# Performance work log

Measured on AMD Instinct MI355X. Metric: run time of the kernel, lower is better.

## Reference

```python
import jax, jax.numpy as jnp
import numpy as np

B, N, DIM, H, HD, COND, BS = 2, 1024, 768, 12, 64, 128, 16
S = 2 * N  # noised tokens [0:N) concatenated with clean x0 tokens [N:2N)
EPS = 1e-5
NEG = -1e30


def setup_inputs() -> dict:
    key = jax.random.key(0)
    ks = jax.random.split(key, 8)
    d = {}
    d['x'] = jax.random.normal(ks[0], (B, S, DIM), jnp.float32)
    d['c'] = jax.random.normal(ks[1], (B, COND), jnp.float32)
    # Rotary table for positions 0..N-1 (each half of the 2N sequence reuses the same positions)
    inv_freq = 1.0 / (10000.0 ** (np.arange(0, HD, 2, dtype=np.float64) / HD))
    freqs = np.arange(N, dtype=np.float64)[:, None] * inv_freq[None, :]
    emb = np.concatenate([freqs, freqs], axis=-1)  # [N, HD]
    cos = np.tile(np.cos(emb), (2, 1))[None, :, None, None, :]
    sin = np.tile(np.sin(emb), (2, 1))[None, :, None, None, :]
    d['cos'] = jnp.asarray(cos, jnp.float32)
    d['sin'] = jnp.asarray(sin, jnp.float32)
    # block-causal diffusion mask (flex_attention_mask): same (block, x0-flag) OR
    # cross-attention from noised block q>0 to strictly earlier CLEAN (x0) blocks
    idx = np.arange(S)
    fl = (idx >= N).astype(np.int64)
    blk = np.where(fl == 1, (idx - N) // BS, idx // BS)
    same = (blk[:, None] == blk[None, :]) & (fl[:, None] == fl[None, :])
    allowed = (blk[:, None] > 0) & (blk[None, :] < blk[:, None]) & (fl[None, :] == 1)
    d['mask'] = jnp.asarray(same | allowed)
    # parameters (adaLN is zero-init in the source; randomized here so the block is non-trivial)
    w = 0.02
    d['norm1_w'] = jnp.ones((DIM,), jnp.float32)
    d['qkv_w'] = jax.random.normal(ks[2], (3 * DIM, DIM), jnp.float32) * w
    d['attn_out_w'] = jax.random.normal(ks[3], (DIM, DIM), jnp.float32) * w
    d['norm2_w'] = jnp.ones((DIM,), jnp.float32)
    d['mlp_w1'] = jax.random.normal(ks[4], (4 * DIM, DIM), jnp.float32) * w
    d['mlp_b1'] = jnp.zeros((4 * DIM,), jnp.float32)
    d['mlp_w2'] = jax.random.normal(ks[5], (DIM, 4 * DIM), jnp.float32) * w
    d['mlp_b2'] = jnp.zeros((DIM,), jnp.float32)
    d['adaLN_w'] = jax.random.normal(ks[6], (6 * DIM, COND), jnp.float32) * w
    d['adaLN_b'] = jax.random.normal(ks[7], (6 * DIM,), jnp.float32) * w
    return d


def _ln(x, w):
    # F.layer_norm (no bias) followed by learned scale, as in the custom LayerNorm
    mu = x.mean(-1, keepdims=True)
    xc = x - mu
    var = (xc * xc).mean(-1, keepdims=True)
    return xc * jax.lax.rsqrt(var + EPS) * w


def reference(x, c, cos, sin, mask, norm1_w, qkv_w, attn_out_w, norm2_w,
              mlp_w1, mlp_b1, mlp_w2, mlp_b2, adaLN_w, adaLN_b):
    # adaLN modulation: [B, 6*DIM] -> six [B, 1, DIM] chunks
    mods = c @ adaLN_w.T + adaLN_b
    (shift_msa, scale_msa, gate_msa,
     shift_mlp, scale_mlp, gate_mlp) = jnp.split(mods[:, None, :], 6, axis=-1)
    x_skip = x
    h = _ln(x, norm1_w) * (1.0 + scale_msa) + shift_msa  # modulate_fused
    # qkv projection + rotary (torchscript path: qkv*cos + rotate_half(qkv)*sin)
    qkv = (h @ qkv_w.T).reshape(x.shape[0], S, 3, H, HD)
    rot = jnp.concatenate([-qkv[..., HD // 2:], qkv[..., :HD // 2]], axis=-1)
    qkv = qkv * cos + rot * sin
    q, k, v = qkv[:, :, 0], qkv[:, :, 1], qkv[:, :, 2]
    # SDPA with the block-causal diffusion mask, scale 1/sqrt(head_dim)
    scores = jnp.einsum('bqhd,bkhd->bhqk', q, k) / np.sqrt(HD).astype(np.float32)
    scores = jnp.where(mask[None, None], scores, NEG)
    p = jax.nn.softmax(scores, axis=-1)
    a = jnp.einsum('bhqk,bkhd->bqhd', p, v).reshape(x.shape[0], S, DIM)
    # bias_dropout_add_scale (inference => no dropout): gate * attn_out + residual
    x = gate_msa * (a @ attn_out_w.T) + x_skip
    h2 = _ln(x, norm2_w) * (1.0 + scale_mlp) + shift_mlp
    m = jax.nn.gelu(h2 @ mlp_w1.T + mlp_b1, approximate=True) @ mlp_w2.T + mlp_b2
    return x + gate_mlp * m
```

## Files before the change

### kernel.cpp

```cpp
#include <hip/hip_runtime.h>
#include <hip/hip_bf16.h>

#define EPS 1e-5f

typedef __attribute__((ext_vector_type(8))) short bf16x8;
typedef __attribute__((ext_vector_type(4))) short bf16x4;
typedef __attribute__((ext_vector_type(4))) float f32x4;

__device__ __forceinline__ f32x4 mfma_bf16(bf16x8 a, bf16x8 b, f32x4 c) {
    return __builtin_amdgcn_mfma_f32_16x16x32_bf16(a, b, c, 0, 0, 0);
}

__device__ __forceinline__ void async_ld16(const void* g, void* l) {
    __builtin_amdgcn_global_load_lds(
        (const __attribute__((address_space(1))) void*)g,
        (__attribute__((address_space(3))) void*)l, 16, 0, 0);
}

__device__ __forceinline__ float fast_gelu(float v) {
    float z2 = 1.5957691216057308f * (v + 0.044715f * v * v * v);
    float e = __expf(z2);
    return v * e / (e + 1.f);
}

__device__ __forceinline__ float bf2f(short s) {
    union { float f; unsigned u; } v;
    v.u = ((unsigned)(unsigned short)s) << 16;
    return v.f;
}

__global__ void k_pre(const float* __restrict__ a, __hip_bfloat16* __restrict__ oa, int na,
                      const float* __restrict__ b, __hip_bfloat16* __restrict__ ob, int nb,
                      const float* __restrict__ c, __hip_bfloat16* __restrict__ oc, int nc,
                      const float* __restrict__ d, __hip_bfloat16* __restrict__ od, int nd,
                      const float* __restrict__ cond, const float* __restrict__ alw,
                      const float* __restrict__ alb, float* __restrict__ mods) {
    if (blockIdx.x >= 27648) {
        int i = (blockIdx.x - 27648) * 256 + threadIdx.x;
        int bb = i / 4608, row = i - bb * 4608;
        const float4* cv = (const float4*)(cond + bb * 128);
        const float4* wv = (const float4*)(alw + (long)row * 128);
        float acc = 0.f;
#pragma unroll
        for (int k = 0; k < 32; ++k) {
            float4 x = cv[k], y = wv[k];
            acc += x.x * y.x + x.y * y.y + x.z * y.z + x.w * y.w;
        }
        mods[i] = acc + alb[row];
        return;
    }
    int i = blockIdx.x * 256 + threadIdx.x;
    if (i < na) { oa[i] = __float2bfloat16(a[i]); return; }
    i -= na;
    if (i < nb) { ob[i] = __float2bfloat16(b[i]); return; }
    i -= nb;
    if (i < nc) { oc[i] = __float2bfloat16(c[i]); return; }
    i -= nc;
    if (i < nd) od[i] = __float2bfloat16(d[i]);
}

__global__ void k_ln_mod(const float* __restrict__ x, const float* __restrict__ w,
                         const float* __restrict__ mods, int shiftOff, int scaleOff,
                         __hip_bfloat16* __restrict__ out) {
    int token = blockIdx.x;
    int lane = threadIdx.x;
    const float4* xr = (const float4*)(x + (long)token * 768);
    float4 v0 = xr[lane], v1 = xr[lane + 64], v2 = xr[lane + 128];
    float s  = v0.x + v0.y + v0.z + v0.w + v1.x + v1.y + v1.z + v1.w + v2.x + v2.y + v2.z + v2.w;
    float ss = v0.x*v0.x + v0.y*v0.y + v0.z*v0.z + v0.w*v0.w
             + v1.x*v1.x + v1.y*v1.y + v1.z*v1.z + v1.w*v1.w
             + v2.x*v2.x + v2.y*v2.y + v2.z*v2.z + v2.w*v2.w;
#pragma unroll
    for (int m = 32; m >= 1; m >>= 1) { s += __shfl_xor(s, m); ss += __shfl_xor(ss, m); }
    float mu = s * (1.f / 768.f);
    float var = ss * (1.f / 768.f) - mu * mu;
    float rs = rsqrtf(var + EPS);
    int b = token >> 11;
    const float* sh = mods + b * 4608 + shiftOff;
    const float* sc = mods + b * 4608 + scaleOff;
    __hip_bfloat16* o = out + (long)token * 768;
    float4 vv[3] = {v0, v1, v2};
#pragma unroll
    for (int kk = 0; kk < 3; ++kk) {
        int cbase = (lane + 64 * kk) * 4;
        const float* p = (const float*)&vv[kk];
#pragma unroll
        for (int j = 0; j < 4; ++j) {
            int col = cbase + j;
            float hv = (p[j] - mu) * rs * w[col] * (1.f + sc[col]) + sh[col];
            o[col] = __float2bfloat16(hv);
        }
    }
}

__global__ void k_red(const __hip_bfloat16* __restrict__ p, const float* __restrict__ x2,
                      const float* __restrict__ mods, const float* __restrict__ bias,
                      float* __restrict__ out) {
    long base = ((long)blockIdx.x * 256 + threadIdx.x) * 4;
    int col = (int)(base % 768);
    int row = (int)(base / 768);
    int b = row >> 11;
    short4 a0 = *(const short4*)(p + base);
    short4 a1 = *(const short4*)(p + 3145728 + base);
    float4 xr = *(const float4*)(x2 + base);
    float4 gt = *(const float4*)(mods + b * 4608 + 3840 + col);
    float4 bs = *(const float4*)(bias + col);
    float4 o;
    o.x = xr.x + gt.x * (bf2f(a0.x) + bf2f(a1.x) + bs.x);
    o.y = xr.y + gt.y * (bf2f(a0.y) + bf2f(a1.y) + bs.y);
    o.z = xr.z + gt.z * (bf2f(a0.z) + bf2f(a1.z) + bs.z);
    o.w = xr.w + gt.w * (bf2f(a0.w) + bf2f(a1.w) + bs.w);
    *(float4*)(out + base) = o;
}

__global__ __launch_bounds__(256) void k_attn(
    const __hip_bfloat16* __restrict__ q, const __hip_bfloat16* __restrict__ k,
    const __hip_bfloat16* __restrict__ vT, __hip_bfloat16* __restrict__ out) {
    __shared__ __hip_bfloat16 pbuf[4][640];
    int wave = threadIdx.x >> 6;
    int lane = threadIdx.x & 63;
    int l15 = lane & 15, quad = lane >> 4;
    int bh = blockIdx.x >> 5;
    int pp = blockIdx.x & 31;
    int fl, blk;
    if      (wave == 0) { fl = 0; blk = 2 * pp; }
    else if (wave == 1) { fl = 0; blk = 2 * pp + 1; }
    else if (wave == 2) { fl = 1; blk = 63 - 2 * pp; }
    else                { fl = 1; blk = 62 - 2 * pp; }
    int qblk = fl * 64 + blk;

    const __hip_bfloat16* Q = q + ((long)bh * 2048 + qblk * 16) * 64;
    bf16x8 qa = *(const bf16x8*)(Q + l15 * 64 + quad * 8);
    bf16x8 qb = *(const bf16x8*)(Q + l15 * 64 + 32 + quad * 8);
    const __hip_bfloat16* K = k + (long)bh * 2048 * 64;
    const __hip_bfloat16* V = vT + (long)bh * 64 * 2048;
    __hip_bfloat16* P = &pbuf[wave][0];

    const f32x4 vzero = {0.f, 0.f, 0.f, 0.f};
    f32x4 o[4]; float l[4];
#pragma unroll
    for (int r = 0; r < 4; ++r) { o[r] = vzero; l[r] = 0.f; }

    int plen = (blk + fl) * 16;
    int nch = (plen + 31) >> 5;
    int total = nch + (fl ? 0 : 1);

    int kbase = (0 < nch) ? 1024 : blk * 16;
    bool v1 = (0 < nch) && (16 < plen);
    bf16x8 ka, kb, k1a, k1b;
    {
        const __hip_bfloat16* K0 = K + (long)kbase * 64;
        ka = *(const bf16x8*)(K0 + l15 * 64 + quad * 8);
        kb = *(const bf16x8*)(K0 + l15 * 64 + 32 + quad * 8);
        k1a = ka; k1b = kb;
        if (v1) {
            const __hip_bfloat16* K1 = K0 + 16 * 64;
            k1a = *(const bf16x8*)(K1 + l15 * 64 + quad * 8);
            k1b = *(const bf16x8*)(K1 + l15 * 64 + 32 + quad * 8);
        }
    }

    for (int ci = 0; ci < total; ++ci) {
        bf16x8 vf[4];
#pragma unroll
        for (int tt = 0; tt < 4; ++tt)
            vf[tt] = *(const bf16x8*)(V + (long)(tt * 16 + l15) * 2048 + kbase + quad * 8);

        f32x4 s0 = mfma_bf16(qb, kb, mfma_bf16(qa, ka, vzero));
        f32x4 s1 = vzero;
        if (v1) s1 = mfma_bf16(qb, k1b, mfma_bf16(qa, k1a, vzero));

        bool hasNext = (ci + 1) < total;
        int nkbase = kbase; bool nv1 = false;
        bf16x8 nka = ka, nkb = kb, nk1a = ka, nk1b = kb;
        if (hasNext) {
            nkbase = (ci + 1 < nch) ? 1024 + (ci + 1) * 32 : blk * 16;
            nv1 = (ci + 1 < nch) && ((ci + 1) * 32 + 16) < plen;
            const __hip_bfloat16* K0 = K + (long)nkbase * 64;
            nka = *(const bf16x8*)(K0 + l15 * 64 + quad * 8);
            nkb = *(const bf16x8*)(K0 + l15 * 64 + 32 + quad * 8);
            if (nv1) {
                const __hip_bfloat16* K1 = K0 + 16 * 64;
                nk1a = *(const bf16x8*)(K1 + l15 * 64 + quad * 8);
                nk1b = *(const bf16x8*)(K1 + l15 * 64 + 32 + quad * 8);
            }
        }

        float p0[4], p1[4];
#pragma unroll
        for (int r = 0; r < 4; ++r) p0[r] = __expf(s0[r]);
        if (v1) {
#pragma unroll
            for (int r = 0; r < 4; ++r) p1[r] = __expf(s1[r]);
        } else {
#pragma unroll
            for (int r = 0; r < 4; ++r) p1[r] = 0.f;
        }
#pragma unroll
        for (int r = 0; r < 4; ++r) {
            l[r] += p0[r] + p1[r];
            int row = quad * 4 + r;
            P[row * 36 + l15]      = __float2bfloat16(p0[r]);
            P[row * 36 + 16 + l15] = __float2bfloat16(p1[r]);
        }
        asm volatile("s_waitcnt lgkmcnt(0)" ::: "memory");
        union { bf16x4 h[2]; bf16x8 v; } u;
        u.h[0] = *(const bf16x4*)(P + l15 * 36 + quad * 8);
        u.h[1] = *(const bf16x4*)(P + l15 * 36 + quad * 8 + 4);
        bf16x8 pa = u.v;
#pragma unroll
        for (int tt = 0; tt < 4; ++tt) o[tt] = mfma_bf16(pa, vf[tt], o[tt]);
        asm volatile("s_waitcnt lgkmcnt(0)" ::: "memory");

        kbase = nkbase; v1 = nv1;
        ka = nka; kb = nkb; k1a = nk1a; k1b = nk1b;
    }

    int b = bh / 12, h = bh - b * 12;
    int seqbase = qblk * 16;
#pragma unroll
    for (int r = 0; r < 4; ++r) {
        float lr = l[r];
#pragma unroll
        for (int msk = 1; msk < 16; msk <<= 1) lr += __shfl_xor(lr, msk, 16);
        float inv = 1.f / lr;
        long row = b * 2048 + seqbase + quad * 4 + r;
#pragma unroll
        for (int tt = 0; tt < 4; ++tt)
            out[row * 768 + h * 64 + tt * 16 + l15] = __float2bfloat16(o[tt][r] * inv);
    }
}

__global__ __launch_bounds__(128) void k_gemm64(
    const __hip_bfloat16* __restrict__ A, const __hip_bfloat16* __restrict__ W,
    __hip_bfloat16* __restrict__ Cb, const float* __restrict__ bias,
    int M, int N, int K) {
    __shared__ __hip_bfloat16 lA[4][64 * 32];
    __shared__ __hip_bfloat16 lB[4][64 * 32];
    int t = threadIdx.x;
    int wave = t >> 6, lane = t & 63, l15 = lane & 15, quad = lane >> 4;
    int sw8 = (quad ^ ((l15 >> 1) & 3)) * 8;
    long bm = blockIdx.x, bn = blockIdx.y;
    const __hip_bfloat16* Ab = A + bm * 64 * K;
    const __hip_bfloat16* Wb = W + bn * 64 * K;

    long soff[2];
#pragma unroll
    for (int call = 0; call < 2; ++call) {
        int chunk = call * 128 + t;
        int row = chunk >> 2;
        int c = (chunk & 3) ^ ((row >> 1) & 3);
        soff[call] = (long)row * K + c * 8;
    }
    auto stage = [&](int k0, int buf) {
        char* lAc = (char*)&lA[buf][0];
        char* lBc = (char*)&lB[buf][0];
#pragma unroll
        for (int call = 0; call < 2; ++call) {
            async_ld16(Ab + soff[call] + k0, lAc + call * 2048 + wave * 1024);
            async_ld16(Wb + soff[call] + k0, lBc + call * 2048 + wave * 1024);
        }
    };

    f32x4 acc[2][4];
#pragma unroll
    for (int i = 0; i < 2; ++i)
#pragma unroll
        for (int j = 0; j < 4; ++j) acc[i][j] = (f32x4){0.f, 0.f, 0.f, 0.f};

    int nIter = K / 32;
    stage(0, 0);
    stage(32, 1);
    stage(64, 2);
    for (int i = 0; i < nIter; ++i) {
        int cb = i & 3;
        if (i > 0) asm volatile("s_barrier" ::: "memory");
        if (i + 3 < nIter) {
            stage((i + 3) * 32, (i + 3) & 3);
            asm volatile("s_waitcnt vmcnt(12)" ::: "memory");
        } else if (i + 3 == nIter) {
            asm volatile("s_waitcnt vmcnt(8)" ::: "memory");
        } else if (i + 2 == nIter) {
            asm volatile("s_waitcnt vmcnt(4)" ::: "memory");
        } else {
            asm volatile("s_waitcnt vmcnt(0)" ::: "memory");
        }
        asm volatile("s_barrier" ::: "memory");
        bf16x8 af[2], bfr[4];
#pragma unroll
        for (int ii = 0; ii < 2; ++ii)
            af[ii] = *(const bf16x8*)&lA[cb][(wave * 32 + ii * 16 + l15) * 32 + sw8];
#pragma unroll
        for (int j = 0; j < 4; ++j)
            bfr[j] = *(const bf16x8*)&lB[cb][(j * 16 + l15) * 32 + sw8];
#pragma unroll
        for (int ii = 0; ii < 2; ++ii)
#pragma unroll
            for (int j = 0; j < 4; ++j)
                acc[ii][j] = mfma_bf16(af[ii], bfr[j], acc[ii][j]);
    }

#pragma unroll
    for (int i = 0; i < 2; ++i) {
#pragma unroll
        for (int j = 0; j < 4; ++j) {
#pragma unroll
            for (int r = 0; r < 4; ++r) {
                int row = (int)bm * 64 + wave * 32 + i * 16 + quad * 4 + r;
                int col = (int)bn * 64 + j * 16 + l15;
                float v = acc[i][j][r] + bias[col];
                Cb[(long)row * N + col] = __float2bfloat16(fast_gelu(v));
            }
        }
    }
}

template <int MODE, int TN>
__global__ __launch_bounds__(TN == 128 ? 256 : 128) void k_gemm(
    const __hip_bfloat16* __restrict__ A, const __hip_bfloat16* __restrict__ W,
    float* __restrict__ Cf, __hip_bfloat16* __restrict__ Cb,
    const float* __restrict__ bias, const float* __restrict__ mods, int gateOff,
    const float* __restrict__ resid, const float* __restrict__ cosb,
    const float* __restrict__ sinb, __hip_bfloat16* __restrict__ qo,
    __hip_bfloat16* __restrict__ ko, __hip_bfloat16* __restrict__ vo,
    int M, int N, int K, int lda) {
    constexpr int NW = (TN == 128) ? 4 : 2;
    constexpr int ACH = 512 / (NW * 64);
    constexpr int BCH = (TN * 4) / (NW * 64);
    constexpr int NINST = ACH + BCH;
    __shared__ __hip_bfloat16 lA[3][128 * 32];
    __shared__ __hip_bfloat16 lB[3][TN * 32];
    int t = threadIdx.x;
    int wave = t >> 6, lane = t & 63, l15 = lane & 15, quad = lane >> 4;
    int wr = (TN == 128) ? (wave >> 1) : wave;
    int wc = (TN == 128) ? (wave & 1) : 0;
    int sw8 = (quad ^ ((l15 >> 1) & 3)) * 8;
    long bm = blockIdx.x, bn = blockIdx.y;
    const __hip_bfloat16* Ab = A + bm * 128 * lda + (long)blockIdx.z * K;
    const __hip_bfloat16* Wb = W + bn * TN * lda + (long)blockIdx.z * K;

    long soffA[ACH], soffB[BCH];
#pragma unroll
    for (int cc = 0; cc < ACH; ++cc) {
        int chunk = cc * NW * 64 + t;
        int row = chunk >> 2;
        int c = (chunk & 3) ^ ((row >> 1) & 3);
        soffA[cc] = (long)row * lda + c * 8;
    }
#pragma unroll
    for (int cc = 0; cc < BCH; ++cc) {
        int chunk = cc * NW * 64 + t;
        int row = chunk >> 2;
        int c = (chunk & 3) ^ ((row >> 1) & 3);
        soffB[cc] = (long)row * lda + c * 8;
    }
    auto stage = [&](int k0, int buf) {
        char* lAc = (char*)&lA[buf][0];
        char* lBc = (char*)&lB[buf][0];
#pragma unroll
        for (int cc = 0; cc < ACH; ++cc)
            async_ld16(Ab + soffA[cc] + k0, lAc + cc * (NW * 1024) + wave * 1024);
#pragma unroll
        for (int cc = 0; cc < BCH; ++cc)
            async_ld16(Wb + soffB[cc] + k0, lBc + cc * (NW * 1024) + wave * 1024);
    };

    f32x4 acc[4][4];
#pragma unroll
    for (int i = 0; i < 4; ++i)
#pragma unroll
        for (int j = 0; j < 4; ++j) acc[i][j] = (f32x4){0.f, 0.f, 0.f, 0.f};

    int nIter = K / 32;
    stage(0, 0);
    stage(32, 1);
    int cb = 0;
    for (int i = 0; i < nIter; ++i) {
        if (i > 0) asm volatile("s_barrier" ::: "memory");
        if (i + 2 < nIter) {
            int nb = cb + 2; if (nb >= 3) nb -= 3;
            stage((i + 2) * 32, nb);
            asm volatile("s_waitcnt vmcnt(%0)" :: "n"(2 * NINST) : "memory");
        } else if (i + 2 == nIter) {
            asm volatile("s_waitcnt vmcnt(%0)" :: "n"(NINST) : "memory");
        } else {
            asm volatile("s_waitcnt vmcnt(0)" ::: "memory");
        }
        asm volatile("s_barrier" ::: "memory");
        bf16x8 af[4], bfr[4];
#pragma unroll
        for (int ii = 0; ii < 4; ++ii)
            af[ii] = *(const bf16x8*)&lA[cb][(wr * 64 + ii * 16 + l15) * 32 + sw8];
#pragma unroll
        for (int j = 0; j < 4; ++j)
            bfr[j] = *(const bf16x8*)&lB[cb][(wc * 64 + j * 16 + l15) * 32 + sw8];
#pragma unroll
        for (int ii = 0; ii < 4; ++ii)
#pragma unroll
            for (int j = 0; j < 4; ++j)
                acc[ii][j] = mfma_bf16(af[ii], bfr[j], acc[ii][j]);
        ++cb; if (cb >= 3) cb = 0;
    }

    if (MODE == 4) {
        int hcol = (int)bn * 2 + wc;
        int th = hcol / 12, h = hcol % 12;
#pragma unroll
        for (int i = 0; i < 4; ++i) {
#pragma unroll
            for (int r = 0; r < 4; ++r) {
                int row = (int)bm * 128 + wr * 64 + i * 16 + quad * 4 + r;
                int s = row & 2047, b = row >> 11;
                long bh_ = b * 12 + h;
                const float* cbp = cosb + s * 64;
                const float* sbp = sinb + s * 64;
#pragma unroll
                for (int j = 0; j < 2; ++j) {
                    int dh = j * 16 + l15;
                    float a0f = acc[i][j][r], a1f = acc[i][j + 2][r];
                    float o0 = a0f * cbp[dh] - a1f * sbp[dh];
                    float o1 = a1f * cbp[dh + 32] + a0f * sbp[dh + 32];
                    if (th == 0) {
                        __hip_bfloat16* d = qo + (bh_ * 2048 + s) * 64;
                        d[dh]      = __float2bfloat16(o0 * 0.125f);
                        d[dh + 32] = __float2bfloat16(o1 * 0.125f);
                    } else if (th == 1) {
                        __hip_bfloat16* d = ko + (bh_ * 2048 + s) * 64;
                        d[dh]      = __float2bfloat16(o0);
                        d[dh + 32] = __float2bfloat16(o1);
                    } else {
                        __hip_bfloat16* d = vo + bh_ * 64 * 2048 + s;
                        d[(long)dh * 2048]        = __float2bfloat16(o0);
                        d[(long)(dh + 32) * 2048] = __float2bfloat16(o1);
                    }
                }
            }
        }
        return;
    }

#pragma unroll
    for (int i = 0; i < 4; ++i) {
#pragma unroll
        for (int j = 0; j < 4; ++j) {
#pragma unroll
            for (int r = 0; r < 4; ++r) {
                int row = (int)bm * 128 + wr * 64 + i * 16 + quad * 4 + r;
                int col = (int)bn * TN + wc * 64 + j * 16 + l15;
                float v = acc[i][j][r];
                long idx = (long)row * N + col;
                if (MODE == 1) {
                    Cf[idx] = mods[(row >> 11) * 4608 + gateOff + col] * v + resid[idx];
                } else if (MODE == 3) {
                    Cf[idx] = resid[idx] + mods[(row >> 11) * 4608 + gateOff + col] * (v + bias[col]);
                } else {
                    Cb[(long)blockIdx.z * M * N + idx] = __float2bfloat16(v);
                }
            }
        }
    }
}

extern "C" void kernel_launch(void* const* d_in, const int* in_sizes, int n_in,
                              void* d_out, int out_size, void* d_ws, size_t ws_size,
                              hipStream_t stream) {
    const float* x    = (const float*)d_in[0];
    const float* c    = (const float*)d_in[1];
    const float* cosb = (const float*)d_in[2];
    const float* sinb = (const float*)d_in[3];
    const float* n1w  = (const float*)d_in[5];
    const float* qkvw = (const float*)d_in[6];
    const float* aow  = (const float*)d_in[7];
    const float* n2w  = (const float*)d_in[8];
    const float* w1   = (const float*)d_in[9];
    const float* b1   = (const float*)d_in[10];
    const float* w2   = (const float*)d_in[11];
    const float* b2   = (const float*)d_in[12];
    const float* alw  = (const float*)d_in[13];
    const float* alb  = (const float*)d_in[14];

    char* ws = (char*)d_ws;
    size_t off = 0;
    auto alloc = [&](size_t bytes) -> void* {
        void* p = ws + off;
        off += (bytes + 255) & ~(size_t)255;
        return p;
    };
    float*          mods = (float*)alloc(2 * 4608 * 4);
    __hip_bfloat16* hbuf = (__hip_bfloat16*)alloc((size_t)4096 * 768 * 2);
    __hip_bfloat16* qb   = (__hip_bfloat16*)alloc((size_t)24 * 2048 * 64 * 2);
    __hip_bfloat16* kb   = (__hip_bfloat16*)alloc((size_t)24 * 2048 * 64 * 2);
    __hip_bfloat16* vT   = (__hip_bfloat16*)alloc((size_t)24 * 64 * 2048 * 2);
    __hip_bfloat16* abuf = (__hip_bfloat16*)alloc((size_t)4096 * 768 * 2);
    float*          x2   = (float*)alloc((size_t)4096 * 768 * 4);
    __hip_bfloat16* h2   = (__hip_bfloat16*)alloc((size_t)4096 * 768 * 2);
    __hip_bfloat16* m1   = (__hip_bfloat16*)alloc((size_t)4096 * 3072 * 2);
    __hip_bfloat16* m2p  = (__hip_bfloat16*)alloc((size_t)2 * 4096 * 768 * 2);
    __hip_bfloat16* wq   = (__hip_bfloat16*)alloc((size_t)2304 * 768 * 2);
    __hip_bfloat16* wa   = (__hip_bfloat16*)alloc((size_t)768 * 768 * 2);
    __hip_bfloat16* w1b  = (__hip_bfloat16*)alloc((size_t)3072 * 768 * 2);
    __hip_bfloat16* w2b  = (__hip_bfloat16*)alloc((size_t)768 * 3072 * 2);

    k_pre<<<27684, 256, 0, stream>>>(qkvw, wq, 2304 * 768, aow, wa, 768 * 768,
                                     w1, w1b, 3072 * 768, w2, w2b, 768 * 3072,
                                     c, alw, alb, mods);
    k_ln_mod<<<4096, 64, 0, stream>>>(x, n1w, mods, 0, 768, hbuf);
    k_gemm<4, 128><<<dim3(32, 18), 256, 0, stream>>>(hbuf, wq, nullptr, nullptr, nullptr, nullptr, 0,
                                                     nullptr, cosb, sinb, qb, kb, vT,
                                                     4096, 2304, 768, 768);
    k_attn<<<768, 256, 0, stream>>>(qb, kb, vT, abuf);
    k_gemm<1, 64><<<dim3(32, 12), 128, 0, stream>>>(abuf, wa, x2, nullptr, nullptr, mods, 1536,
                                                    x, nullptr, nullptr, nullptr, nullptr, nullptr,
                                                    4096, 768, 768, 768);
    k_ln_mod<<<4096, 64, 0, stream>>>(x2, n2w, mods, 2304, 3072, h2);
    k_gemm64<<<dim3(64, 48), 128, 0, stream>>>(h2, w1b, m1, b1, 4096, 3072, 768);
    k_gemm<5, 128><<<dim3(32, 6, 2), 256, 0, stream>>>(m1, w2b, nullptr, m2p, nullptr, nullptr, 0,
                                                       nullptr, nullptr, nullptr, nullptr, nullptr, nullptr,
                                                       4096, 768, 1536, 3072);
    k_red<<<3072, 256, 0, stream>>>(m2p, x2, mods, b2, (float*)d_out);
}
```

Before: 333.1 us.

## Replace 64x64 MLP-up GEMM with 128x128 tile path and double-buffer pipeline

Drops the dedicated 64x64-tile GELU GEMM kernel and routes the MLP up-projection through the generic 128x128-tile k_gemm via a new MODE 2 epilogue (bias + GELU to bf16). The generic GEMM's LDS pipeline also shrinks from triple to double buffering, with one stage prefetched ahead instead of two. Bigger tiles raise operand reuse and cut global traffic for the 3072-wide GEMM. The shallower prefetch lowers LDS use and may raise occupancy for every GEMM, but it hides less memory latency.

```diff
diff --git a/kernel.cpp b/kernel.cpp
--- a/kernel.cpp
+++ b/kernel.cpp
@@ -231,90 +231,6 @@
     }
 }
 
-__global__ __launch_bounds__(128) void k_gemm64(
-    const __hip_bfloat16* __restrict__ A, const __hip_bfloat16* __restrict__ W,
-    __hip_bfloat16* __restrict__ Cb, const float* __restrict__ bias,
-    int M, int N, int K) {
-    __shared__ __hip_bfloat16 lA[4][64 * 32];
-    __shared__ __hip_bfloat16 lB[4][64 * 32];
-    int t = threadIdx.x;
-    int wave = t >> 6, lane = t & 63, l15 = lane & 15, quad = lane >> 4;
-    int sw8 = (quad ^ ((l15 >> 1) & 3)) * 8;
-    long bm = blockIdx.x, bn = blockIdx.y;
-    const __hip_bfloat16* Ab = A + bm * 64 * K;
-    const __hip_bfloat16* Wb = W + bn * 64 * K;
-
-    long soff[2];
-#pragma unroll
-    for (int call = 0; call < 2; ++call) {
-        int chunk = call * 128 + t;
-        int row = chunk >> 2;
-        int c = (chunk & 3) ^ ((row >> 1) & 3);
-        soff[call] = (long)row * K + c * 8;
-    }
-    auto stage = [&](int k0, int buf) {
-        char* lAc = (char*)&lA[buf][0];
-        char* lBc = (char*)&lB[buf][0];
-#pragma unroll
-        for (int call = 0; call < 2; ++call) {
-            async_ld16(Ab + soff[call] + k0, lAc + call * 2048 + wave * 1024);
-            async_ld16(Wb + soff[call] + k0, lBc + call * 2048 + wave * 1024);
-        }
-    };
-
-    f32x4 acc[2][4];
-#pragma unroll
-    for (int i = 0; i < 2; ++i)
-#pragma unroll
-        for (int j = 0; j < 4; ++j) acc[i][j] = (f32x4){0.f, 0.f, 0.f, 0.f};
-
-    int nIter = K / 32;
-    stage(0, 0);
-    stage(32, 1);
-    stage(64, 2);
-    for (int i = 0; i < nIter; ++i) {
-        int cb = i & 3;
-        if (i > 0) asm volatile("s_barrier" ::: "memory");
-        if (i + 3 < nIter) {
-            stage((i + 3) * 32, (i + 3) & 3);
-            asm volatile("s_waitcnt vmcnt(12)" ::: "memory");
-        } else if (i + 3 == nIter) {
-            asm volatile("s_waitcnt vmcnt(8)" ::: "memory");
-        } else if (i + 2 == nIter) {
-            asm volatile("s_waitcnt vmcnt(4)" ::: "memory");
-        } else {
-            asm volatile("s_waitcnt vmcnt(0)" ::: "memory");
-        }
-        asm volatile("s_barrier" ::: "memory");
-        bf16x8 af[2], bfr[4];
-#pragma unroll
-        for (int ii = 0; ii < 2; ++ii)
-            af[ii] = *(const bf16x8*)&lA[cb][(wave * 32 + ii * 16 + l15) * 32 + sw8];
-#pragma unroll
-        for (int j = 0; j < 4; ++j)
-            bfr[j] = *(const bf16x8*)&lB[cb][(j * 16 + l15) * 32 + sw8];
-#pragma unroll
-        for (int ii = 0; ii < 2; ++ii)
-#pragma unroll
-            for (int j = 0; j < 4; ++j)
-                acc[ii][j] = mfma_bf16(af[ii], bfr[j], acc[ii][j]);
-    }
-
-#pragma unroll
-    for (int i = 0; i < 2; ++i) {
-#pragma unroll
-        for (int j = 0; j < 4; ++j) {
-#pragma unroll
-            for (int r = 0; r < 4; ++r) {
-                int row = (int)bm * 64 + wave * 32 + i * 16 + quad * 4 + r;
-                int col = (int)bn * 64 + j * 16 + l15;
-                float v = acc[i][j][r] + bias[col];
-                Cb[(long)row * N + col] = __float2bfloat16(fast_gelu(v));
-            }
-        }
-    }
-}
-
 template <int MODE, int TN>
 __global__ __launch_bounds__(TN == 128 ? 256 : 128) void k_gemm(
     const __hip_bfloat16* __restrict__ A, const __hip_bfloat16* __restrict__ W,
@@ -328,8 +244,8 @@
     constexpr int ACH = 512 / (NW * 64);
     constexpr int BCH = (TN * 4) / (NW * 64);
     constexpr int NINST = ACH + BCH;
-    __shared__ __hip_bfloat16 lA[3][128 * 32];
-    __shared__ __hip_bfloat16 lB[3][TN * 32];
+    __shared__ __hip_bfloat16 lA[2][128 * 32];
+    __shared__ __hip_bfloat16 lB[2][TN * 32];
     int t = threadIdx.x;
     int wave = t >> 6, lane = t & 63, l15 = lane & 15, quad = lane >> 4;
     int wr = (TN == 128) ? (wave >> 1) : wave;
@@ -373,15 +289,11 @@
 
     int nIter = K / 32;
     stage(0, 0);
-    stage(32, 1);
-    int cb = 0;
     for (int i = 0; i < nIter; ++i) {
+        int cb = i & 1;
         if (i > 0) asm volatile("s_barrier" ::: "memory");
-        if (i + 2 < nIter) {
-            int nb = cb + 2; if (nb >= 3) nb -= 3;
-            stage((i + 2) * 32, nb);
-            asm volatile("s_waitcnt vmcnt(%0)" :: "n"(2 * NINST) : "memory");
-        } else if (i + 2 == nIter) {
+        if (i + 1 < nIter) {
+            stage((i + 1) * 32, cb ^ 1);
             asm volatile("s_waitcnt vmcnt(%0)" :: "n"(NINST) : "memory");
         } else {
             asm volatile("s_waitcnt vmcnt(0)" ::: "memory");
@@ -399,7 +311,6 @@
 #pragma unroll
             for (int j = 0; j < 4; ++j)
                 acc[ii][j] = mfma_bf16(af[ii], bfr[j], acc[ii][j]);
-        ++cb; if (cb >= 3) cb = 0;
     }
 
     if (MODE == 4) {
@@ -451,6 +362,8 @@
                 long idx = (long)row * N + col;
                 if (MODE == 1) {
                     Cf[idx] = mods[(row >> 11) * 4608 + gateOff + col] * v + resid[idx];
+                } else if (MODE == 2) {
+                    Cb[idx] = __float2bfloat16(fast_gelu(v + bias[col]));
                 } else if (MODE == 3) {
                     Cf[idx] = resid[idx] + mods[(row >> 11) * 4608 + gateOff + col] * (v + bias[col]);
                 } else {
@@ -513,7 +426,9 @@
                                                     x, nullptr, nullptr, nullptr, nullptr, nullptr,
                                                     4096, 768, 768, 768);
     k_ln_mod<<<4096, 64, 0, stream>>>(x2, n2w, mods, 2304, 3072, h2);
-    k_gemm64<<<dim3(64, 48), 128, 0, stream>>>(h2, w1b, m1, b1, 4096, 3072, 768);
+    k_gemm<2, 128><<<dim3(32, 24), 256, 0, stream>>>(h2, w1b, nullptr, m1, b1, nullptr, 0,
+                                                     nullptr, nullptr, nullptr, nullptr, nullptr, nullptr,
+                                                     4096, 3072, 768, 768);
     k_gemm<5, 128><<<dim3(32, 6, 2), 256, 0, stream>>>(m1, w2b, nullptr, m2p, nullptr, nullptr, 0,
                                                        nullptr, nullptr, nullptr, nullptr, nullptr, nullptr,
                                                        4096, 768, 1536, 3072);
```

After: 314.4 us. 1.06x faster.
